# Kernel tuning notes

Measured on AMD Instinct MI355X. Metric: run time of the kernel, lower is better.

Reference implementation:

```python
import jax, jax.numpy as jnp
import numpy as np

B, S, D, H = 2, 2048, 1024, 16
HD = D // H  # head_dim = 64


def setup_inputs() -> dict:
    key = jax.random.key(0)
    ks = jax.random.split(key, 6)
    scale_h = 1.0 / np.sqrt(HD)
    scale_d = 1.0 / np.sqrt(D)
    return {
        "x": jax.random.normal(ks[0], (B, S, D), dtype=jnp.float32),
        # per-head projection weights (CausalAttention Linear(head_dim, head_dim, bias=False)), stacked over heads
        "Wq": jax.random.normal(ks[1], (H, HD, HD), dtype=jnp.float32) * scale_h,
        "Wk": jax.random.normal(ks[2], (H, HD, HD), dtype=jnp.float32) * scale_h,
        "Wv": jax.random.normal(ks[3], (H, HD, HD), dtype=jnp.float32) * scale_h,
        # final nn.Linear(dim, dim): y = x @ Wo + bo (Wo stored already transposed vs torch)
        "Wo": jax.random.normal(ks[4], (D, D), dtype=jnp.float32) * scale_d,
        "bo": jax.random.normal(ks[5], (D,), dtype=jnp.float32) * 0.01,
    }


def reference(x, Wq, Wk, Wv, Wo, bo):
    b, s, d = x.shape
    h, hd, _ = Wq.shape
    # head h sees contiguous channel slice x[:, :, h*hd:(h+1)*hd]
    xh = x.reshape(b, s, h, hd)                                  # [B,S,H,HD]
    q = jnp.einsum("bshd,hde->bhse", xh, Wq)                     # [B,H,S,HD]
    k = jnp.einsum("bshd,hde->bhse", xh, Wk)
    v = jnp.einsum("bshd,hde->bhse", xh, Wv)
    scores = jnp.einsum("bhse,bhte->bhst", q, k) * (hd ** -0.5)  # [B,H,S,S]
    causal = jnp.tril(jnp.ones((s, s), dtype=bool))
    scores = jnp.where(causal, scores, jnp.finfo(scores.dtype).min)
    attn = jax.nn.softmax(scores, axis=-1)
    out = jnp.einsum("bhst,bhtd->bshd", attn, v)                 # [B,S,H,HD]
    # torch.stack(out_list, dim=-1) -> [B,S,HD,H]; reshape -> interleaved channels
    out = jnp.swapaxes(out, -1, -2).reshape(b, s, d)
    return out @ Wo + bo
```

## Files before the change

### kernel.cpp

```cpp
#include <hip/hip_runtime.h>

typedef __attribute__((ext_vector_type(8))) _Float16 half8;
typedef __attribute__((ext_vector_type(2))) __fp16 fp16x2;
typedef __attribute__((ext_vector_type(4))) float f32x4;
typedef __attribute__((ext_vector_type(16))) float f32x16;

constexpr int Bc = 2, Sc = 2048, Dc = 1024, Hc = 16, HDc = 64;

__device__ __forceinline__ int swz(int row, int colh) {
  return row * 64 + (colh ^ ((row & 7) * 8));
}

#define PKU(a, b) __builtin_bit_cast(unsigned, __builtin_amdgcn_cvt_pkrtz((a), (b)))

#define PACK_STORE(vA0, vA1, vA2, vA3, vB0, vB1, vB2, vB3, ptr) {        \
  unsigned W0 = PKU(vA0, vA1), W1 = PKU(vA2, vA3);                       \
  unsigned X0 = PKU(vB0, vB1), X1 = PKU(vB2, vB3);                       \
  unsigned s0_ = (unsigned)__shfl_xor((int)(hi ? W0 : X0), 32);          \
  unsigned s1_ = (unsigned)__shfl_xor((int)(hi ? W1 : X1), 32);          \
  union { unsigned u[4]; half8 h8; } P_;                                 \
  P_.u[0] = hi ? s0_ : W0; P_.u[1] = hi ? s1_ : W1;                      \
  P_.u[2] = hi ? X0 : s0_; P_.u[3] = hi ? X1 : s1_;                      \
  *(half8*)(ptr) = P_.h8; }

__global__ __launch_bounds__(256) void prep_w(const float* __restrict__ Wq,
                                              const float* __restrict__ Wk,
                                              const float* __restrict__ Wv,
                                              _Float16* __restrict__ WT) {
  const int m = blockIdx.x >> 4;
  const int h = blockIdx.x & 15;
  const float* src = (m == 0 ? Wq : (m == 1 ? Wk : Wv)) + (size_t)h * 4096;
  const float scale = (m == 0) ? 0.125f * 1.44269504088896f : 1.0f;
  __shared__ float T[64][65];
  const int tid = threadIdx.x;
#pragma unroll
  for (int i = 0; i < 4; ++i) {
    int r = (tid >> 4) + 16 * i, c4 = (tid & 15) * 4;
    *(float4*)&T[r][c4] = *(const float4*)(src + r * 64 + c4);
  }
  __syncthreads();
  _Float16* dst = WT + ((size_t)m * 16 + h) * 4096;
#pragma unroll
  for (int i = 0; i < 4; ++i) {
    int e = (tid >> 4) + 16 * i, d4 = (tid & 15) * 4;
    union { _Float16 hh[4]; unsigned long long u; } pk;
#pragma unroll
    for (int j = 0; j < 4; ++j) pk.hh[j] = (_Float16)(T[d4 + j][e] * scale);
    *(unsigned long long*)(dst + (size_t)e * 64 + d4) = pk.u;
  }
}

__global__ __launch_bounds__(256) void prep_wo(const float* __restrict__ Wo,
                                               _Float16* __restrict__ WoT) {
  __shared__ float T[64][68];
  const int hh = blockIdx.x;
  const int n0 = blockIdx.y * 64;
  const int tid = threadIdx.x;
#pragma unroll
  for (int i = 0; i < 4; ++i) {
    int g = tid + i * 256;
    int e = g >> 4, c4 = (g & 15) * 4;
    *(float4*)&T[e][c4] = *(const float4*)(Wo + (size_t)(e * 16 + hh) * Dc + n0 + c4);
  }
  __syncthreads();
#pragma unroll
  for (int i = 0; i < 4; ++i) {
    int g = tid + i * 256;
    int c = g >> 4, e4 = (g & 15) * 4;
    union { _Float16 h[4]; unsigned long long u; } pk;
    pk.h[0] = (_Float16)T[e4 + 0][c];
    pk.h[1] = (_Float16)T[e4 + 1][c];
    pk.h[2] = (_Float16)T[e4 + 2][c];
    pk.h[3] = (_Float16)T[e4 + 3][c];
    *(unsigned long long*)(WoT + (size_t)(n0 + c) * Dc + hh * 64 + e4) = pk.u;
  }
}

__global__ __launch_bounds__(256) void qkv_proj(
    const float* __restrict__ x, const _Float16* __restrict__ WT,
    _Float16* __restrict__ Qp, _Float16* __restrict__ Kp,
    _Float16* __restrict__ Vp) {
  const int h = blockIdx.x & 15;
  const int st = (blockIdx.x >> 4) & 15;
  const int b = blockIdx.x >> 8;
  const int s0 = st * 128;
  __shared__ __align__(16) _Float16 xs[128 * 64];
  const int tid = threadIdx.x;
#pragma unroll
  for (int i = 0; i < 4; ++i) {
    int r = (tid >> 3) + 32 * i;
    int c8 = (tid & 7) * 8;
    const float* xp = x + ((size_t)(b * Sc + s0 + r)) * Dc + h * 64 + c8;
    float4 u0 = *(const float4*)xp;
    float4 u1 = *(const float4*)(xp + 4);
    union { fp16x2 h2[4]; half8 h8; } pk;
    pk.h2[0] = __builtin_amdgcn_cvt_pkrtz(u0.x, u0.y);
    pk.h2[1] = __builtin_amdgcn_cvt_pkrtz(u0.z, u0.w);
    pk.h2[2] = __builtin_amdgcn_cvt_pkrtz(u1.x, u1.y);
    pk.h2[3] = __builtin_amdgcn_cvt_pkrtz(u1.z, u1.w);
    *(half8*)&xs[swz(r, c8)] = pk.h8;
  }
  __syncthreads();
  const int l = tid & 63, w = tid >> 6;
  const int lq = l & 31, hi = l >> 5;
  half8 xa[4];
#pragma unroll
  for (int c = 0; c < 4; ++c)
    xa[c] = *(const half8*)&xs[swz(32 * w + lq, c * 16 + hi * 8)];

  const _Float16* WTq = WT + (size_t)h * 4096;
  const _Float16* WTk = WT + (size_t)(16 + h) * 4096;
  const _Float16* WTv = WT + (size_t)(32 + h) * 4096;
  f32x16 Qt[2] = {}, Kt[2] = {}, Vd[2] = {};
#pragma unroll
  for (int et = 0; et < 2; ++et) {
#pragma unroll
    for (int c = 0; c < 4; ++c) {
      const int off = (32 * et + lq) * 64 + c * 16 + hi * 8;
      half8 wqf = *(const half8*)(WTq + off);
      half8 wkf = *(const half8*)(WTk + off);
      half8 wvf = *(const half8*)(WTv + off);
      Qt[et] = __builtin_amdgcn_mfma_f32_32x32x16_f16(wqf, xa[c], Qt[et], 0, 0, 0);
      Kt[et] = __builtin_amdgcn_mfma_f32_32x32x16_f16(wkf, xa[c], Kt[et], 0, 0, 0);
      Vd[et] = __builtin_amdgcn_mfma_f32_32x32x16_f16(xa[c], wvf, Vd[et], 0, 0, 0);
    }
  }
  const int bh = b * Hc + h;
  const int qt_ = 4 * st + w;
  const int ktile = 2 * st + (w >> 1);
  _Float16* qdst = Qp + (((size_t)(bh * 64 + qt_) * 4) << 9) + (l << 3);
  _Float16* kdst = Kp + (((size_t)((bh * 32 + ktile) * 8) + (w & 1) * 4) << 9) + (l << 3);
  _Float16* vdst = Vp + (((size_t)(bh * 32 + ktile) * 8) << 9) + (l << 3);

  PACK_STORE(Qt[0][0], Qt[0][1], Qt[0][2], Qt[0][3], Qt[0][4], Qt[0][5], Qt[0][6], Qt[0][7], qdst + (0 << 9));
  PACK_STORE(Qt[0][8], Qt[0][9], Qt[0][10], Qt[0][11], Qt[0][12], Qt[0][13], Qt[0][14], Qt[0][15], qdst + (1 << 9));
  PACK_STORE(Qt[1][0], Qt[1][1], Qt[1][2], Qt[1][3], Qt[1][4], Qt[1][5], Qt[1][6], Qt[1][7], qdst + (2 << 9));
  PACK_STORE(Qt[1][8], Qt[1][9], Qt[1][10], Qt[1][11], Qt[1][12], Qt[1][13], Qt[1][14], Qt[1][15], qdst + (3 << 9));

  PACK_STORE(Kt[0][0], Kt[0][1], Kt[0][2], Kt[0][3], Kt[0][4], Kt[0][5], Kt[0][6], Kt[0][7], kdst + (0 << 9));
  PACK_STORE(Kt[0][8], Kt[0][9], Kt[0][10], Kt[0][11], Kt[0][12], Kt[0][13], Kt[0][14], Kt[0][15], kdst + (1 << 9));
  PACK_STORE(Kt[1][0], Kt[1][1], Kt[1][2], Kt[1][3], Kt[1][4], Kt[1][5], Kt[1][6], Kt[1][7], kdst + (2 << 9));
  PACK_STORE(Kt[1][8], Kt[1][9], Kt[1][10], Kt[1][11], Kt[1][12], Kt[1][13], Kt[1][14], Kt[1][15], kdst + (3 << 9));

#pragma unroll
  for (int et = 0; et < 2; ++et) {
    PACK_STORE(Vd[et][0], Vd[et][1], Vd[et][2], Vd[et][3], Vd[et][4], Vd[et][5], Vd[et][6], Vd[et][7],
               vdst + ((size_t)(et * 4 + ((2 * w + 0) & 3)) << 9));
    PACK_STORE(Vd[et][8], Vd[et][9], Vd[et][10], Vd[et][11], Vd[et][12], Vd[et][13], Vd[et][14], Vd[et][15],
               vdst + ((size_t)(et * 4 + ((2 * w + 1) & 3)) << 9));
  }
}

__global__ __launch_bounds__(64, 2) void flash_attn(
    const _Float16* __restrict__ Qp, const _Float16* __restrict__ Kp,
    const _Float16* __restrict__ Vp, _Float16* __restrict__ attC) {
  const int i = blockIdx.x;
  const int xcd = i & 7, j = i >> 3;
  const int bh = xcd * 4 + (j & 3);
  const int qt = 63 - (j >> 2);
  const int q0 = qt * 32;
  const int NT = qt / 2 + 1;
  const int b = bh >> 4, h = bh & 15;
  const int l = threadIdx.x, lq = l & 31, hi = l >> 5;
  const int q_global = q0 + lq;
  const size_t kvb = (size_t)bh * 32;

  const _Float16* qb = Qp + (((size_t)(bh * 64 + qt) * 4) << 9) + (l << 3);
  half8 qf[4];
#pragma unroll
  for (int c = 0; c < 4; ++c) qf[c] = *(const half8*)(qb + (c << 9));

  f32x16 OA = {}, OB = {};
  float m_run = -1e30f, l_run = 0.f;
  half8 kaE[4], kbE[4], kaO[4], kbO[4];

#define DOB(t) (((t) * 64 + 32) <= q0 + 31)

#define LOADK(KA, KB, t) {                                                    \
  const _Float16* p8 = Kp + (((kvb + (t)) * 8) << 9) + (l << 3);              \
  _Pragma("unroll") for (int c = 0; c < 4; ++c)                               \
    KA[c] = *(const half8*)(p8 + (c << 9));                                   \
  if (DOB(t)) {                                                               \
    _Pragma("unroll") for (int c = 0; c < 4; ++c)                             \
      KB[c] = *(const half8*)(p8 + ((4 + c) << 9));                           \
  } }

#define STEP(KA, KB, t) {                                                     \
  const int k0 = (t) * 64;                                                    \
  const bool doB = DOB(t);                                                    \
  const _Float16* vp8 = Vp + (((kvb + (t)) * 8) << 9) + (l << 3);             \
  half8 va[4], vb[4];                                                         \
  _Pragma("unroll") for (int c = 0; c < 4; ++c) {                             \
    va[c] = *(const half8*)(vp8 + (c << 9));                                  \
    vb[c] = *(const half8*)(vp8 + ((4 + c) << 9));                            \
  }                                                                           \
  f32x16 SA = {}, SB = {};                                                    \
  __builtin_amdgcn_s_setprio(1);                                              \
  _Pragma("unroll") for (int c = 0; c < 4; ++c)                               \
    SA = __builtin_amdgcn_mfma_f32_32x32x16_f16(KA[c], qf[c], SA, 0, 0, 0);   \
  if (doB) {                                                                  \
    _Pragma("unroll") for (int c = 0; c < 4; ++c)                             \
      SB = __builtin_amdgcn_mfma_f32_32x32x16_f16(KB[c], qf[c], SB, 0, 0, 0); \
  }                                                                           \
  __builtin_amdgcn_s_setprio(0);                                              \
  if (k0 + 63 > q0) {                                                         \
    _Pragma("unroll") for (int r = 0; r < 16; ++r) {                          \
      const int kk = k0 + (r & 3) + 8 * (r >> 2) + 4 * hi;                    \
      if (kk > q_global) SA[r] = -1e30f;                                      \
      if (doB && kk + 32 > q_global) SB[r] = -1e30f;                          \
    }                                                                         \
  }                                                                           \
  float mx = -1e30f;                                                          \
  _Pragma("unroll") for (int r = 0; r < 16; ++r) mx = fmaxf(mx, SA[r]);       \
  if (doB) {                                                                  \
    _Pragma("unroll") for (int r = 0; r < 16; ++r) mx = fmaxf(mx, SB[r]);     \
  }                                                                           \
  mx = fmaxf(mx, __shfl_xor(mx, 32));                                         \
  if (!__all(mx <= m_run + 4.0f)) {                                           \
    const float mnew = fmaxf(m_run, mx);                                      \
    const float corr = __builtin_amdgcn_exp2f(m_run - mnew);                  \
    l_run *= corr;                                                            \
    _Pragma("unroll") for (int r = 0; r < 16; ++r) { OA[r] *= corr; OB[r] *= corr; } \
    m_run = mnew;                                                             \
  }                                                                           \
  float Pv[32];                                                               \
  float ls = 0.f;                                                             \
  _Pragma("unroll") for (int r = 0; r < 16; ++r) {                            \
    Pv[r] = __builtin_amdgcn_exp2f(SA[r] - m_run);                            \
    ls += Pv[r];                                                              \
  }                                                                           \
  if (doB) {                                                                  \
    _Pragma("unroll") for (int r = 0; r < 16; ++r) {                          \
      Pv[16 + r] = __builtin_amdgcn_exp2f(SB[r] - m_run);                     \
      ls += Pv[16 + r];                                                       \
    }                                                                         \
  }                                                                           \
  ls += __shfl_xor(ls, 32);                                                   \
  l_run += ls;                                                                \
  __builtin_amdgcn_s_setprio(1);                                              \
  _Pragma("unroll") for (int ch = 0; ch < 4; ++ch) {                          \
    if (ch < (doB ? 4 : 2)) {                                                 \
      unsigned W0 = PKU(Pv[ch * 8 + 0], Pv[ch * 8 + 1]);                      \
      unsigned W1 = PKU(Pv[ch * 8 + 2], Pv[ch * 8 + 3]);                      \
      unsigned W2 = PKU(Pv[ch * 8 + 4], Pv[ch * 8 + 5]);                      \
      unsigned W3 = PKU(Pv[ch * 8 + 6], Pv[ch * 8 + 7]);                      \
      unsigned sw0 = (unsigned)__shfl_xor((int)(hi ? W0 : W2), 32);           \
      unsigned sw1 = (unsigned)__shfl_xor((int)(hi ? W1 : W3), 32);           \
      union { unsigned u[4]; half8 h; } pa;                                   \
      pa.u[0] = hi ? sw0 : W0;                                                \
      pa.u[1] = hi ? sw1 : W1;                                                \
      pa.u[2] = hi ? W2 : sw0;                                                \
      pa.u[3] = hi ? W3 : sw1;                                                \
      OA = __builtin_amdgcn_mfma_f32_32x32x16_f16(va[ch], pa.h, OA, 0, 0, 0); \
      OB = __builtin_amdgcn_mfma_f32_32x32x16_f16(vb[ch], pa.h, OB, 0, 0, 0); \
    }                                                                         \
  }                                                                           \
  __builtin_amdgcn_s_setprio(0); }

  LOADK(kaE, kbE, 0);
  int kt = 0;
  for (; kt + 2 <= NT; kt += 2) {
    LOADK(kaO, kbO, kt + 1);
    STEP(kaE, kbE, kt);
    if (kt + 2 < NT) { LOADK(kaE, kbE, kt + 2); }
    STEP(kaO, kbO, kt + 1);
  }
  if (kt < NT) { STEP(kaE, kbE, kt); }

  const float inv = 1.f / l_run;
  _Float16* op = attC + ((size_t)b * Sc + q_global) * Dc + h * 64;
#pragma unroll
  for (int g = 0; g < 4; ++g) {
    union { _Float16 hh[4]; unsigned long long u; } pA, pB;
#pragma unroll
    for (int jj = 0; jj < 4; ++jj) {
      pA.hh[jj] = (_Float16)(OA[4 * g + jj] * inv);
      pB.hh[jj] = (_Float16)(OB[4 * g + jj] * inv);
    }
    *(unsigned long long*)(op + 8 * g + 4 * hi) = pA.u;
    *(unsigned long long*)(op + 32 + 8 * g + 4 * hi) = pB.u;
  }
}

__global__ __launch_bounds__(256) void out_proj(
    const _Float16* __restrict__ attC, const _Float16* __restrict__ WoT,
    const float* __restrict__ bo, float* __restrict__ out) {
  const int m0 = blockIdx.x * 128, n0 = blockIdx.y * 128;
  __shared__ __align__(16) _Float16 Alds[128][32];
  __shared__ __align__(16) _Float16 Blds[128][32];
  const int tid = threadIdx.x;
  const int l = tid & 63, w = tid >> 6;
  const int wm = w >> 1, wn = w & 1;
  const int lr = l & 15, lg = l >> 4;
  f32x4 acc[4][4] = {};
  for (int kt = 0; kt < 32; ++kt) {
    const int k0 = kt * 32;
#pragma unroll
    for (int i = 0; i < 2; ++i) {
      int g = tid + i * 256;
      int r = g >> 2, c8 = (g & 3) * 8;
      *(half8*)&Alds[r][c8] = *(const half8*)(attC + (size_t)(m0 + r) * Dc + k0 + c8);
      *(half8*)&Blds[r][c8] = *(const half8*)(WoT + (size_t)(n0 + r) * Dc + k0 + c8);
    }
    __syncthreads();
    half8 af[4], bf[4];
#pragma unroll
    for (int i2 = 0; i2 < 4; ++i2) {
      af[i2] = *(const half8*)&Alds[wm * 64 + i2 * 16 + lr][lg * 8];
      bf[i2] = *(const half8*)&Blds[wn * 64 + i2 * 16 + lr][lg * 8];
    }
#pragma unroll
    for (int am = 0; am < 4; ++am)
#pragma unroll
      for (int bn = 0; bn < 4; ++bn)
        acc[am][bn] = __builtin_amdgcn_mfma_f32_16x16x32_f16(af[am], bf[bn], acc[am][bn], 0, 0, 0);
    __syncthreads();
  }
#pragma unroll
  for (int am = 0; am < 4; ++am)
#pragma unroll
    for (int bn = 0; bn < 4; ++bn) {
      int n = n0 + wn * 64 + bn * 16 + lr;
      float bias = bo[n];
#pragma unroll
      for (int r = 0; r < 4; ++r) {
        int m = m0 + wm * 64 + am * 16 + lg * 4 + r;
        out[(size_t)m * Dc + n] = acc[am][bn][r] + bias;
      }
    }
}

extern "C" void kernel_launch(void* const* d_in, const int* in_sizes, int n_in,
                              void* d_out, int out_size, void* d_ws, size_t ws_size,
                              hipStream_t stream) {
  const float* x  = (const float*)d_in[0];
  const float* Wq = (const float*)d_in[1];
  const float* Wk = (const float*)d_in[2];
  const float* Wv = (const float*)d_in[3];
  const float* Wo = (const float*)d_in[4];
  const float* bo = (const float*)d_in[5];
  float* out = (float*)d_out;
  char* ws = (char*)d_ws;
  _Float16* Qp   = (_Float16*)(ws);
  _Float16* Kp   = (_Float16*)(ws + (size_t)(8  << 20));
  _Float16* Vp   = (_Float16*)(ws + (size_t)(16 << 20));
  _Float16* WoT  = (_Float16*)(ws + (size_t)(24 << 20));
  _Float16* WT   = (_Float16*)(ws + (size_t)(26 << 20));
  _Float16* attC = (_Float16*)(ws + (size_t)(26 << 20));

  prep_w<<<dim3(48), dim3(256), 0, stream>>>(Wq, Wk, Wv, WT);
  prep_wo<<<dim3(16, 16), dim3(256), 0, stream>>>(Wo, WoT);
  qkv_proj<<<dim3(512), dim3(256), 0, stream>>>(x, WT, Qp, Kp, Vp);
  flash_attn<<<dim3(2048), dim3(64), 0, stream>>>(Qp, Kp, Vp, attC);
  out_proj<<<dim3(32, 8), dim3(256), 0, stream>>>(attC, WoT, bo, out);
}
```

Measured before the change: 88.72 us.

## Pair long/short query tiles per block with split-KV merge; shrink out_proj tiles

Flash attention now launches 1024 two-wave blocks. Each block pairs a long causal query tile with its mirror short tile. Wave 0 handles the first 16 KV tiles of the long tile, and wave 1 handles the short tile and then the remaining KV tiles of the long tile. The two partial softmax states are merged through shared memory. This balances causal work within a block and reduces tail imbalance, at the cost of a sync, a shared-memory merge and reloading Q. Separately, out_proj uses 64x128 tiles with padded LDS rows, which doubles the grid for better occupancy and reduces bank conflicts.

```diff
diff --git a/kernel.cpp b/kernel.cpp
--- a/kernel.cpp
+++ b/kernel.cpp
@@ -151,43 +151,21 @@
   }
 }
 
-__global__ __launch_bounds__(64, 2) void flash_attn(
-    const _Float16* __restrict__ Qp, const _Float16* __restrict__ Kp,
-    const _Float16* __restrict__ Vp, _Float16* __restrict__ attC) {
-  const int i = blockIdx.x;
-  const int xcd = i & 7, j = i >> 3;
-  const int bh = xcd * 4 + (j & 3);
-  const int qt = 63 - (j >> 2);
-  const int q0 = qt * 32;
-  const int NT = qt / 2 + 1;
-  const int b = bh >> 4, h = bh & 15;
-  const int l = threadIdx.x, lq = l & 31, hi = l >> 5;
-  const int q_global = q0 + lq;
-  const size_t kvb = (size_t)bh * 32;
-
-  const _Float16* qb = Qp + (((size_t)(bh * 64 + qt) * 4) << 9) + (l << 3);
-  half8 qf[4];
-#pragma unroll
-  for (int c = 0; c < 4; ++c) qf[c] = *(const half8*)(qb + (c << 9));
-
-  f32x16 OA = {}, OB = {};
-  float m_run = -1e30f, l_run = 0.f;
-  half8 kaE[4], kbE[4], kaO[4], kbO[4];
-
-#define DOB(t) (((t) * 64 + 32) <= q0 + 31)
-
-#define LOADK(KA, KB, t) {                                                    \
+#define DOB(t, q0v) (((t) * 64 + 32) <= (q0v) + 31)
+
+#define LOADK(KA, KB, t, q0v) {                                               \
   const _Float16* p8 = Kp + (((kvb + (t)) * 8) << 9) + (l << 3);              \
   _Pragma("unroll") for (int c = 0; c < 4; ++c)                               \
     KA[c] = *(const half8*)(p8 + (c << 9));                                   \
-  if (DOB(t)) {                                                               \
+  if (DOB(t, q0v)) {                                                          \
     _Pragma("unroll") for (int c = 0; c < 4; ++c)                             \
       KB[c] = *(const half8*)(p8 + ((4 + c) << 9));                           \
   } }
 
-#define STEP(KA, KB, t) {                                                     \
+#define STEP(KA, KB, t, q0v) {                                                \
   const int k0 = (t) * 64;                                                    \
-  const bool doB = DOB(t);                                                    \
+  const bool doB = DOB(t, q0v);                                               \
+  const int q_g = (q0v) + lq;                                                 \
   const _Float16* vp8 = Vp + (((kvb + (t)) * 8) << 9) + (l << 3);             \
   half8 va[4], vb[4];                                                         \
   _Pragma("unroll") for (int c = 0; c < 4; ++c) {                             \
@@ -203,11 +181,11 @@
       SB = __builtin_amdgcn_mfma_f32_32x32x16_f16(KB[c], qf[c], SB, 0, 0, 0); \
   }                                                                           \
   __builtin_amdgcn_s_setprio(0);                                              \
-  if (k0 + 63 > q0) {                                                         \
+  if (k0 + 63 > (q0v)) {                                                      \
     _Pragma("unroll") for (int r = 0; r < 16; ++r) {                          \
       const int kk = k0 + (r & 3) + 8 * (r >> 2) + 4 * hi;                    \
-      if (kk > q_global) SA[r] = -1e30f;                                      \
-      if (doB && kk + 32 > q_global) SB[r] = -1e30f;                          \
+      if (kk > q_g) SA[r] = -1e30f;                                           \
+      if (doB && kk + 32 > q_g) SB[r] = -1e30f;                               \
     }                                                                         \
   }                                                                           \
   float mx = -1e30f;                                                          \
@@ -257,75 +235,157 @@
   }                                                                           \
   __builtin_amdgcn_s_setprio(0); }
 
-  LOADK(kaE, kbE, 0);
-  int kt = 0;
-  for (; kt + 2 <= NT; kt += 2) {
-    LOADK(kaO, kbO, kt + 1);
-    STEP(kaE, kbE, kt);
-    if (kt + 2 < NT) { LOADK(kaE, kbE, kt + 2); }
-    STEP(kaO, kbO, kt + 1);
-  }
-  if (kt < NT) { STEP(kaE, kbE, kt); }
-
-  const float inv = 1.f / l_run;
-  _Float16* op = attC + ((size_t)b * Sc + q_global) * Dc + h * 64;
-#pragma unroll
-  for (int g = 0; g < 4; ++g) {
-    union { _Float16 hh[4]; unsigned long long u; } pA, pB;
-#pragma unroll
-    for (int jj = 0; jj < 4; ++jj) {
-      pA.hh[jj] = (_Float16)(OA[4 * g + jj] * inv);
-      pB.hh[jj] = (_Float16)(OB[4 * g + jj] * inv);
-    }
-    *(unsigned long long*)(op + 8 * g + 4 * hi) = pA.u;
-    *(unsigned long long*)(op + 32 + 8 * g + 4 * hi) = pB.u;
+#define RUN_RANGE(t0, t1, q0v) {                                              \
+  int t = (t0);                                                               \
+  LOADK(kaE, kbE, t, q0v);                                                    \
+  for (; t + 2 <= (t1); t += 2) {                                             \
+    LOADK(kaO, kbO, t + 1, q0v);                                              \
+    STEP(kaE, kbE, t, q0v);                                                   \
+    if (t + 2 < (t1)) { LOADK(kaE, kbE, t + 2, q0v); }                        \
+    STEP(kaO, kbO, t + 1, q0v);                                               \
+  }                                                                           \
+  if (t < (t1)) { STEP(kaE, kbE, t, q0v); } }
+
+__global__ __launch_bounds__(128, 2) void flash_attn(
+    const _Float16* __restrict__ Qp, const _Float16* __restrict__ Kp,
+    const _Float16* __restrict__ Vp, _Float16* __restrict__ attC) {
+  const int i = blockIdx.x;
+  const int bh = (i & 7) * 4 + ((i >> 3) & 3);
+  const int p = i >> 5;
+  const int qlong = 63 - p, qshort = p;
+  const int NTL = qlong / 2 + 1;
+  const int b = bh >> 4, h = bh & 15;
+  const int tid = threadIdx.x;
+  const int wv = tid >> 6, l = tid & 63;
+  const int lq = l & 31, hi = l >> 5;
+  const size_t kvb = (size_t)bh * 32;
+
+  __shared__ __align__(16) float Osh[8][64][4];
+  __shared__ float mlsh[2][64];
+
+  half8 qf[4], kaE[4], kbE[4], kaO[4], kbO[4];
+  f32x16 OA = {}, OB = {};
+  float m_run = -1e30f, l_run = 0.f;
+
+  if (wv == 0) {
+    const int q0 = qlong * 32;
+    const _Float16* qb = Qp + (((size_t)(bh * 64 + qlong) * 4) << 9) + (l << 3);
+#pragma unroll
+    for (int c = 0; c < 4; ++c) qf[c] = *(const half8*)(qb + (c << 9));
+    RUN_RANGE(0, 16, q0);
+  } else {
+    const int q0s = qshort * 32;
+    const int NTS = qshort / 2 + 1;
+    const _Float16* qb = Qp + (((size_t)(bh * 64 + qshort) * 4) << 9) + (l << 3);
+#pragma unroll
+    for (int c = 0; c < 4; ++c) qf[c] = *(const half8*)(qb + (c << 9));
+    RUN_RANGE(0, NTS, q0s);
+    {
+      const float inv = 1.f / l_run;
+      _Float16* op = attC + ((size_t)b * Sc + q0s + lq) * Dc + h * 64;
+#pragma unroll
+      for (int g = 0; g < 4; ++g) {
+        union { _Float16 hh[4]; unsigned long long u; } pA, pB;
+#pragma unroll
+        for (int jj = 0; jj < 4; ++jj) {
+          pA.hh[jj] = (_Float16)(OA[4 * g + jj] * inv);
+          pB.hh[jj] = (_Float16)(OB[4 * g + jj] * inv);
+        }
+        *(unsigned long long*)(op + 8 * g + 4 * hi) = pA.u;
+        *(unsigned long long*)(op + 32 + 8 * g + 4 * hi) = pB.u;
+      }
+    }
+    const int q0 = qlong * 32;
+    const _Float16* qb2 = Qp + (((size_t)(bh * 64 + qlong) * 4) << 9) + (l << 3);
+#pragma unroll
+    for (int c = 0; c < 4; ++c) qf[c] = *(const half8*)(qb2 + (c << 9));
+#pragma unroll
+    for (int r = 0; r < 16; ++r) { OA[r] = 0.f; OB[r] = 0.f; }
+    m_run = -1e30f; l_run = 0.f;
+    RUN_RANGE(16, NTL, q0);
+#pragma unroll
+    for (int g = 0; g < 4; ++g) {
+      float4 a, bq;
+      a.x = OA[4 * g + 0]; a.y = OA[4 * g + 1]; a.z = OA[4 * g + 2]; a.w = OA[4 * g + 3];
+      bq.x = OB[4 * g + 0]; bq.y = OB[4 * g + 1]; bq.z = OB[4 * g + 2]; bq.w = OB[4 * g + 3];
+      *(float4*)&Osh[g][l][0] = a;
+      *(float4*)&Osh[4 + g][l][0] = bq;
+    }
+    mlsh[0][l] = m_run;
+    mlsh[1][l] = l_run;
+  }
+  __syncthreads();
+  if (wv == 0) {
+    const float m1 = mlsh[0][l], l1 = mlsh[1][l];
+    const float mm = fmaxf(m_run, m1);
+    const float c0 = __builtin_amdgcn_exp2f(m_run - mm);
+    const float c1 = __builtin_amdgcn_exp2f(m1 - mm);
+    const float linv = 1.f / (l_run * c0 + l1 * c1);
+    _Float16* op = attC + ((size_t)b * Sc + qlong * 32 + lq) * Dc + h * 64;
+#pragma unroll
+    for (int g = 0; g < 4; ++g) {
+      const float4 o1a = *(const float4*)&Osh[g][l][0];
+      const float4 o1b = *(const float4*)&Osh[4 + g][l][0];
+      union { _Float16 hh[4]; unsigned long long u; } pA, pB;
+      pA.hh[0] = (_Float16)((OA[4 * g + 0] * c0 + o1a.x * c1) * linv);
+      pA.hh[1] = (_Float16)((OA[4 * g + 1] * c0 + o1a.y * c1) * linv);
+      pA.hh[2] = (_Float16)((OA[4 * g + 2] * c0 + o1a.z * c1) * linv);
+      pA.hh[3] = (_Float16)((OA[4 * g + 3] * c0 + o1a.w * c1) * linv);
+      pB.hh[0] = (_Float16)((OB[4 * g + 0] * c0 + o1b.x * c1) * linv);
+      pB.hh[1] = (_Float16)((OB[4 * g + 1] * c0 + o1b.y * c1) * linv);
+      pB.hh[2] = (_Float16)((OB[4 * g + 2] * c0 + o1b.z * c1) * linv);
+      pB.hh[3] = (_Float16)((OB[4 * g + 3] * c0 + o1b.w * c1) * linv);
+      *(unsigned long long*)(op + 8 * g + 4 * hi) = pA.u;
+      *(unsigned long long*)(op + 32 + 8 * g + 4 * hi) = pB.u;
+    }
   }
 }
 
 __global__ __launch_bounds__(256) void out_proj(
     const _Float16* __restrict__ attC, const _Float16* __restrict__ WoT,
     const float* __restrict__ bo, float* __restrict__ out) {
-  const int m0 = blockIdx.x * 128, n0 = blockIdx.y * 128;
-  __shared__ __align__(16) _Float16 Alds[128][32];
-  __shared__ __align__(16) _Float16 Blds[128][32];
+  const int m0 = blockIdx.x * 64, n0 = blockIdx.y * 128;
+  __shared__ __align__(16) _Float16 Alds[64][40];
+  __shared__ __align__(16) _Float16 Blds[128][40];
   const int tid = threadIdx.x;
   const int l = tid & 63, w = tid >> 6;
-  const int wm = w >> 1, wn = w & 1;
   const int lr = l & 15, lg = l >> 4;
-  f32x4 acc[4][4] = {};
+  f32x4 acc[4][2] = {};
   for (int kt = 0; kt < 32; ++kt) {
     const int k0 = kt * 32;
-#pragma unroll
-    for (int i = 0; i < 2; ++i) {
-      int g = tid + i * 256;
-      int r = g >> 2, c8 = (g & 3) * 8;
+    {
+      const int r = tid >> 2, c8 = (tid & 3) * 8;
       *(half8*)&Alds[r][c8] = *(const half8*)(attC + (size_t)(m0 + r) * Dc + k0 + c8);
-      *(half8*)&Blds[r][c8] = *(const half8*)(WoT + (size_t)(n0 + r) * Dc + k0 + c8);
+#pragma unroll
+      for (int ii = 0; ii < 2; ++ii) {
+        const int g = tid + ii * 256;
+        const int rb = g >> 2, cb = (g & 3) * 8;
+        *(half8*)&Blds[rb][cb] = *(const half8*)(WoT + (size_t)(n0 + rb) * Dc + k0 + cb);
+      }
     }
     __syncthreads();
-    half8 af[4], bf[4];
-#pragma unroll
-    for (int i2 = 0; i2 < 4; ++i2) {
-      af[i2] = *(const half8*)&Alds[wm * 64 + i2 * 16 + lr][lg * 8];
-      bf[i2] = *(const half8*)&Blds[wn * 64 + i2 * 16 + lr][lg * 8];
-    }
-#pragma unroll
-    for (int am = 0; am < 4; ++am)
-#pragma unroll
-      for (int bn = 0; bn < 4; ++bn)
-        acc[am][bn] = __builtin_amdgcn_mfma_f32_16x16x32_f16(af[am], bf[bn], acc[am][bn], 0, 0, 0);
+    half8 af[4], bf[2];
+#pragma unroll
+    for (int i2 = 0; i2 < 4; ++i2) af[i2] = *(const half8*)&Alds[i2 * 16 + lr][lg * 8];
+#pragma unroll
+    for (int j = 0; j < 2; ++j) bf[j] = *(const half8*)&Blds[w * 32 + j * 16 + lr][lg * 8];
+#pragma unroll
+    for (int i2 = 0; i2 < 4; ++i2)
+#pragma unroll
+      for (int j = 0; j < 2; ++j)
+        acc[i2][j] = __builtin_amdgcn_mfma_f32_16x16x32_f16(af[i2], bf[j], acc[i2][j], 0, 0, 0);
     __syncthreads();
   }
 #pragma unroll
-  for (int am = 0; am < 4; ++am)
-#pragma unroll
-    for (int bn = 0; bn < 4; ++bn) {
-      int n = n0 + wn * 64 + bn * 16 + lr;
-      float bias = bo[n];
+  for (int i2 = 0; i2 < 4; ++i2)
+#pragma unroll
+    for (int j = 0; j < 2; ++j) {
+      const int n = n0 + w * 32 + j * 16 + lr;
+      const float bias = bo[n];
 #pragma unroll
       for (int r = 0; r < 4; ++r) {
-        int m = m0 + wm * 64 + am * 16 + lg * 4 + r;
-        out[(size_t)m * Dc + n] = acc[am][bn][r] + bias;
+        const int m = m0 + i2 * 16 + lg * 4 + r;
+        out[(size_t)m * Dc + n] = acc[i2][j][r] + bias;
       }
     }
 }
@@ -351,6 +411,6 @@
   prep_w<<<dim3(48), dim3(256), 0, stream>>>(Wq, Wk, Wv, WT);
   prep_wo<<<dim3(16, 16), dim3(256), 0, stream>>>(Wo, WoT);
   qkv_proj<<<dim3(512), dim3(256), 0, stream>>>(x, WT, Qp, Kp, Vp);
-  flash_attn<<<dim3(2048), dim3(64), 0, stream>>>(Qp, Kp, Vp, attC);
-  out_proj<<<dim3(32, 8), dim3(256), 0, stream>>>(attC, WoT, bo, out);
-}
+  flash_attn<<<dim3(1024), dim3(128), 0, stream>>>(Qp, Kp, Vp, attC);
+  out_proj<<<dim3(64, 8), dim3(256), 0, stream>>>(attC, WoT, bo, out);
+}
```

New measurement: 79.29 us. 10.6% less time.
